# Kernel tuning notes

Measured on AMD Instinct MI355X. Metric: run time of the kernel, lower is better.

## Reference

```python
import jax, jax.numpy as jnp
import numpy as np

B, T, S, PD = 512, 2048, 16, 4

def setup_inputs() -> dict:
    key = jax.random.key(0)
    ks = jax.random.split(key, 10)
    w = lambda k, sh: (jax.random.normal(k, sh, dtype=jnp.float32) * 0.1)
    return {
        'z': jax.random.normal(ks[0], (B, T, S), dtype=jnp.float32),
        'p': jax.random.normal(ks[1], (B, T, PD), dtype=jnp.float32),
        'mu0': jnp.zeros((B, S), dtype=jnp.float32),
        'P0': jnp.full((B, S), 0.1, dtype=jnp.float32),  # cfg['kf_P0']
        'Wq1': w(ks[2], (PD, 64)), 'bq1': jnp.zeros((64,), jnp.float32),
        'Wq2': w(ks[3], (64, S)),  'bq2': jnp.zeros((S,), jnp.float32),
        'Wr1': w(ks[4], (PD, 64)), 'br1': jnp.zeros((64,), jnp.float32),
        'Wr2': w(ks[5], (64, S)),  'br2': jnp.zeros((S,), jnp.float32),
        'Wg1': w(ks[6], (PD, 32)), 'bg1': jnp.zeros((32,), jnp.float32),
        'Wg2': w(ks[7], (32, 1)),  'bg2': jnp.zeros((1,), jnp.float32),
    }

def _mlp(x, W1, b1, W2, b2):
    return jax.nn.relu(x @ W1 + b1) @ W2 + b2

def reference(z, p, mu0, P0, Wq1, bq1, Wq2, bq2, Wr1, br1, Wr2, br2, Wg1, bg1, Wg2, bg2):
    # z: [B,T,S], p: [B,T,PD]; scan over time with batched Kalman state.
    zT = jnp.swapaxes(z, 0, 1)  # [T,B,S]
    pT = jnp.swapaxes(p, 0, 1)  # [T,B,PD]

    def step(carry, inp):
        mu, P = carry            # [B,S], [B,S]
        z_t, p_t = inp           # [B,S], [B,PD]
        Q_t = jax.nn.softplus(_mlp(p_t, Wq1, bq1, Wq2, bq2)) + 1e-8
        R_t = jax.nn.softplus(_mlp(p_t, Wr1, br1, Wr2, br2)) + 1e-8
        P_pred = P + Q_t
        K = jnp.clip(P_pred / (P_pred + R_t), 1e-6, 0.95)
        gamma_t = jax.nn.sigmoid(_mlp(p_t, Wg1, bg1, Wg2, bg2))  # [B,1] (scalar per sample)
        mu_new = mu + gamma_t * (K * (z_t - mu))
        P_new = (1.0 - K) * P_pred
        return (mu_new, P_new), mu_new

    (mu_f, P_f), mus = jax.lax.scan(step, (mu0, P0), (zT, pT))
    return jnp.swapaxes(mus, 0, 1)  # [B,T,S]
```

## Files before the change

### kernel.cpp

```cpp
#include <hip/hip_runtime.h>
#include <hip/hip_fp16.h>
#include <stdint.h>
#include <math.h>

#define KB 512
#define KT 2048
#define KS 16
#define KPD 4
#define QT 512
#define NQ (KT / QT)
#define QSTR 515
#define HSTR 40

typedef _Float16 f16;
typedef _Float16 f16x8 __attribute__((ext_vector_type(8)));
typedef float f32x4 __attribute__((ext_vector_type(4)));

#define MFMA16(A, B, C) __builtin_amdgcn_mfma_f32_16x16x32_f16(A, B, C, 0, 0, 0)

__device__ __forceinline__ float softplus_f(float x) {
    float ax = fabsf(x);
    float e  = __expf(-ax);
    return fmaxf(x, 0.0f) + __logf(1.0f + e);
}
__device__ __forceinline__ float sigmoid_f(float x) {
    return __builtin_amdgcn_rcpf(1.0f + __expf(-x));
}
__device__ __forceinline__ float h2f_lo(uint32_t w) {
    return __half2float(__ushort_as_half((unsigned short)(w & 0xffffu)));
}
__device__ __forceinline__ float h2f_hi(uint32_t w) {
    return __half2float(__ushort_as_half((unsigned short)(w >> 16)));
}
__device__ __forceinline__ f16x8 zero8() {
    f16x8 v;
#pragma unroll
    for (int i = 0; i < 8; ++i) v[i] = (f16)0;
    return v;
}
__device__ __forceinline__ int spos(int t) { return t ^ ((t >> 5) & 31); }

__device__ __forceinline__ uint32_t pkrelu(float a, float b) {
    auto h = __builtin_amdgcn_cvt_pkrtz(fmaxf(a, 0.f), fmaxf(b, 0.f));
    uint32_t w; __builtin_memcpy(&w, &h, 4);
    return w;
}
__device__ __forceinline__ uint16_t f2h(float x) {
    return (uint16_t)__half_as_ushort(__float2half_rn(x));
}
__device__ __forceinline__ float h2f(uint16_t x) {
    return __half2float(__ushort_as_half((unsigned short)x));
}

__global__ __launch_bounds__(512, 2) void kalman_one(
    const float* __restrict__ z, const float* __restrict__ p,
    const float* __restrict__ mu0, const float* __restrict__ P0,
    const float* __restrict__ Wq1, const float* __restrict__ bq1,
    const float* __restrict__ Wq2, const float* __restrict__ bq2,
    const float* __restrict__ Wr1, const float* __restrict__ br1,
    const float* __restrict__ Wr2, const float* __restrict__ br2,
    const float* __restrict__ Wg1, const float* __restrict__ bg1,
    const float* __restrict__ Wg2, const float* __restrict__ bg2,
    float* __restrict__ out)
{
    __shared__ __align__(16) uint32_t QRl[KS * QSTR];
    __shared__ __align__(16) float    Gl[QT];
    __shared__ __align__(16) uint16_t Hs[8 * KS * HSTR];
    __shared__ __align__(16) uint16_t zsh[KS * QSTR];

    const int tid = threadIdx.x;
    const int wv = tid >> 6;
    const int l = tid & 63;
    const int g = l >> 4;
    const int c = l & 15;
    const int b = blockIdx.x;

    f16* __restrict__ Hw = reinterpret_cast<f16*>(Hs) + wv * (KS * HSTR);

    const float* __restrict__ zb = z + (size_t)b * KT * KS;
    const float* __restrict__ pb = p + (size_t)b * KT * KPD;
    float* __restrict__ ob = out + (size_t)b * KT * KS;

    f16x8 fA1[10];
#pragma unroll
    for (int m = 0; m < 10; ++m) {
        const float* W = (m < 4) ? (Wq1 + m * 16)
                       : (m < 8) ? (Wr1 + (m - 4) * 16)
                                 : (Wg1 + (m - 8) * 16);
        const int ld = (m < 8) ? 64 : 32;
        float w0 = W[0 * ld + c], w1 = W[1 * ld + c],
              w2 = W[2 * ld + c], w3 = W[3 * ld + c];
        f16x8 a = zero8();
        if (g == 0) { a[0] = (f16)w0; a[1] = (f16)w1; a[2] = (f16)w2; a[3] = (f16)w3; }
        fA1[m] = a;
    }
    f16x8 fA2[5];
#pragma unroll
    for (int i = 0; i < 4; ++i) {
        const float* W = (i < 2) ? Wq2 : Wr2;
        const int kb = (i & 1) * 32;
        f16x8 a;
#pragma unroll
        for (int j = 0; j < 8; ++j) a[j] = (f16)W[(kb + g * 8 + j) * 16 + c];
        fA2[i] = a;
    }
    {
        f16x8 a = zero8();
        if (c == 0) {
#pragma unroll
            for (int j = 0; j < 8; ++j) a[j] = (f16)Wg2[g * 8 + j];
        }
        fA2[4] = a;
    }
    const float bQ0 = bq2[g * 4 + 0], bQ1 = bq2[g * 4 + 1],
                bQ2 = bq2[g * 4 + 2], bQ3 = bq2[g * 4 + 3];
    const float bR0 = br2[g * 4 + 0], bR1 = br2[g * 4 + 1],
                bR2 = br2[g * 4 + 2], bR3 = br2[g * 4 + 3];
    const float bG = bg2[0];

    float muA = mu0[b * KS + wv],     PA = P0[b * KS + wv];
    float muB = mu0[b * KS + wv + 8], PB = P0[b * KS + wv + 8];

    auto scan_s = [&](int s, float& mu_q, float& P_q) {
        uint32_t qr[8];
        const uint32_t* qrow = QRl + (size_t)s * QSTR;
        float zvv[8], gvv[8];
#pragma unroll
        for (int i = 0; i < 8; ++i) {
            const int ps = spos(l * 8 + i);
            qr[i] = qrow[ps];
            zvv[i] = h2f(zsh[s * QSTR + ps]);
            gvv[i] = Gl[ps];
        }
        float c00 = 1.f, c01 = 0.f, c10 = 0.f, c11 = 1.f;
#pragma unroll
        for (int i = 0; i < 8; ++i) {
            float Q = h2f_lo(qr[i]), Rr = h2f_hi(qr[i]);
            float ta = fmaf(Q, c10, c00);
            float tb = fmaf(Q, c11, c01);
            float n10 = fmaf(Q + Rr, c10, c00);
            float n11 = fmaf(Q + Rr, c11, c01);
            c00 = Rr * ta; c01 = Rr * tb; c10 = n10; c11 = n11;
        }
        float rn = __builtin_amdgcn_rcpf(c11);
        float ma = c00 * rn, mb = c01 * rn, mc = c10 * rn;
#pragma unroll
        for (int r = 0; r < 6; ++r) {
            const int d = 1 << r;
            float pa = __shfl_up(ma, d);
            float pbv = __shfl_up(mb, d);
            float pc = __shfl_up(mc, d);
            float na = fmaf(ma, pa, mb * pc);
            float nb = fmaf(ma, pbv, mb);
            float nc = fmaf(mc, pa, pc);
            float nd = fmaf(mc, pbv, 1.f);
            float rr = __builtin_amdgcn_rcpf(nd);
            bool act = (l >= d);
            ma = act ? na * rr : ma;
            mb = act ? nb * rr : mb;
            mc = act ? nc * rr : mc;
        }
        float ea = __shfl_up(ma, 1);
        float eb = __shfl_up(mb, 1);
        float ec = __shfl_up(mc, 1);
        if (l == 0) { ea = 1.f; eb = 0.f; ec = 0.f; }
        float P = fmaf(ea, P_q, eb) * __builtin_amdgcn_rcpf(fmaf(ec, P_q, 1.f));

        float av[8], bw[8];
        float A = 1.f, Bv = 0.f;
#pragma unroll
        for (int i = 0; i < 8; ++i) {
            float Q = h2f_lo(qr[i]), Rr = h2f_hi(qr[i]);
            float Pp = P + Q;
            float K0 = Pp * __builtin_amdgcn_rcpf(Pp + Rr);
            float Kk = __builtin_amdgcn_fmed3f(K0, 1e-6f, 0.95f);
            float gk = gvv[i] * Kk;
            av[i] = 1.f - gk;
            bw[i] = gk * zvv[i];
            P = fmaf(-Kk, Pp, Pp);
            A = A * av[i];
            Bv = fmaf(av[i], Bv, bw[i]);
        }
        float P_end = __shfl(P, 63);
#pragma unroll
        for (int r = 0; r < 6; ++r) {
            const int d = 1 << r;
            float pA = __shfl_up(A, d);
            float pB = __shfl_up(Bv, d);
            float nA = A * pA;
            float nB = fmaf(A, pB, Bv);
            bool act = (l >= d);
            A  = act ? nA : A;
            Bv = act ? nB : Bv;
        }
        float eA = __shfl_up(A, 1);
        float eB = __shfl_up(Bv, 1);
        if (l == 0) { eA = 1.f; eB = 0.f; }
        float mu = fmaf(eA, mu_q, eB);
#pragma unroll
        for (int i = 0; i < 8; ++i) {
            mu = fmaf(av[i], mu, bw[i]);
            zsh[s * QSTR + spos(l * 8 + i)] = f2h(mu);
        }
        mu_q = __shfl(mu, 63);
        P_q = P_end;
    };

    for (int q = 0; q < NQ; ++q) {
        {
            const int trow = q * QT + wv * 64;
            const float4 pv = *reinterpret_cast<const float4*>(pb + (size_t)(trow + l) * KPD);

#pragma unroll
            for (int n = 0; n < 4; ++n) {
                f16x8 fBP;
                {
                    const int src = n * 16 + c;
                    float x = __shfl(pv.x, src);
                    float y = __shfl(pv.y, src);
                    float zz = __shfl(pv.z, src);
                    float w = __shfl(pv.w, src);
                    fBP = zero8();
                    if (g == 0) { fBP[0] = (f16)x; fBP[1] = (f16)y; fBP[2] = (f16)zz; fBP[3] = (f16)w; }
                }

                f32x4 aq; aq[0] = bQ0; aq[1] = bQ1; aq[2] = bQ2; aq[3] = bQ3;
                f32x4 ar; ar[0] = bR0; ar[1] = bR1; ar[2] = bR2; ar[3] = bR3;
                f32x4 ag; ag[0] = 0.f; ag[1] = 0.f; ag[2] = 0.f; ag[3] = 0.f;

                uint32_t* Hd = reinterpret_cast<uint32_t*>(Hw);

#pragma unroll
                for (int X = 0; X < 5; ++X) {
                    const int m0 = 2 * X, m1 = 2 * X + 1;
                    {
                        const float* bs = (m0 < 4) ? (bq1 + m0 * 16)
                                        : (m0 < 8) ? (br1 + (m0 - 4) * 16)
                                                   : (bg1 + (m0 - 8) * 16);
                        f32x4 acc;
                        acc[0] = bs[g * 4 + 0]; acc[1] = bs[g * 4 + 1];
                        acc[2] = bs[g * 4 + 2]; acc[3] = bs[g * 4 + 3];
                        acc = MFMA16(fA1[m0], fBP, acc);
                        Hd[c * 20 + g * 2 + 0] = pkrelu(acc[0], acc[1]);
                        Hd[c * 20 + g * 2 + 1] = pkrelu(acc[2], acc[3]);
                    }
                    {
                        const float* bs = (m1 < 4) ? (bq1 + m1 * 16)
                                        : (m1 < 8) ? (br1 + (m1 - 4) * 16)
                                                   : (bg1 + (m1 - 8) * 16);
                        f32x4 acc;
                        acc[0] = bs[g * 4 + 0]; acc[1] = bs[g * 4 + 1];
                        acc[2] = bs[g * 4 + 2]; acc[3] = bs[g * 4 + 3];
                        acc = MFMA16(fA1[m1], fBP, acc);
                        Hd[c * 20 + 8 + g * 2 + 0] = pkrelu(acc[0], acc[1]);
                        Hd[c * 20 + 8 + g * 2 + 1] = pkrelu(acc[2], acc[3]);
                    }
                    f16x8 fb = *reinterpret_cast<const f16x8*>(Hw + c * HSTR + g * 8);
                    if (X == 0)      aq = MFMA16(fA2[0], fb, aq);
                    else if (X == 1) aq = MFMA16(fA2[1], fb, aq);
                    else if (X == 2) ar = MFMA16(fA2[2], fb, ar);
                    else if (X == 3) ar = MFMA16(fA2[3], fb, ar);
                    else             ag = MFMA16(fA2[4], fb, ag);
                }

                const int tt = wv * 64 + n * 16 + c;
                const int ps = spos(tt);
#pragma unroll
                for (int i = 0; i < 4; ++i) {
                    float Qv = softplus_f(aq[i]) + 1e-8f;
                    float Rv = softplus_f(ar[i]) + 1e-8f;
                    auto pk = __builtin_amdgcn_cvt_pkrtz(Qv, Rv);
                    uint32_t w; __builtin_memcpy(&w, &pk, 4);
                    QRl[(size_t)(g * 4 + i) * QSTR + ps] = w;
                }
                if (g == 0)
                    Gl[ps] = sigmoid_f(ag[0] + bG);
            }

            const float4* zq = reinterpret_cast<const float4*>(zb + (size_t)q * QT * KS);
#pragma unroll
            for (int v = 0; v < 4; ++v) {
                int k = tid + 512 * v;
                float4 w = zq[k];
                int t = k >> 2, s0 = (k & 3) << 2;
                const int ps = spos(t);
                zsh[(s0 + 0) * QSTR + ps] = f2h(w.x);
                zsh[(s0 + 1) * QSTR + ps] = f2h(w.y);
                zsh[(s0 + 2) * QSTR + ps] = f2h(w.z);
                zsh[(s0 + 3) * QSTR + ps] = f2h(w.w);
            }
        }
        __syncthreads();

        scan_s(wv, muA, PA);
        scan_s(wv + 8, muB, PB);
        __syncthreads();

        {
            float* od = ob + (size_t)q * QT * KS;
#pragma unroll
            for (int v = 0; v < 4; ++v) {
                int k = tid + 512 * v;
                int t = k >> 2, s0 = (k & 3) << 2;
                const int ps = spos(t);
                float4 w;
                w.x = h2f(zsh[(s0 + 0) * QSTR + ps]);
                w.y = h2f(zsh[(s0 + 1) * QSTR + ps]);
                w.z = h2f(zsh[(s0 + 2) * QSTR + ps]);
                w.w = h2f(zsh[(s0 + 3) * QSTR + ps]);
                *reinterpret_cast<float4*>(od + 4 * (size_t)k) = w;
            }
        }
        __syncthreads();
    }
}

extern "C" void kernel_launch(void* const* d_in, const int* in_sizes, int n_in,
                              void* d_out, int out_size, void* d_ws, size_t ws_size,
                              hipStream_t stream) {
    const float* z   = (const float*)d_in[0];
    const float* p   = (const float*)d_in[1];
    const float* mu0 = (const float*)d_in[2];
    const float* P0  = (const float*)d_in[3];
    const float* Wq1 = (const float*)d_in[4];
    const float* bq1 = (const float*)d_in[5];
    const float* Wq2 = (const float*)d_in[6];
    const float* bq2 = (const float*)d_in[7];
    const float* Wr1 = (const float*)d_in[8];
    const float* br1 = (const float*)d_in[9];
    const float* Wr2 = (const float*)d_in[10];
    const float* br2 = (const float*)d_in[11];
    const float* Wg1 = (const float*)d_in[12];
    const float* bg1 = (const float*)d_in[13];
    const float* Wg2 = (const float*)d_in[14];
    const float* bg2 = (const float*)d_in[15];
    float* out = (float*)d_out;

    hipLaunchKernelGGL(kalman_one, dim3(KB), dim3(512), 0, stream,
                       z, p, mu0, P0, Wq1, bq1, Wq2, bq2,
                       Wr1, br1, Wr2, br2, Wg1, bg1, Wg2, bg2, out);
}
```

Baseline: 86.88 us.

## Add higher-occupancy kalman_fast kernel with LDS-staged MFMA weights and spill check

Adds a new kernel variant with launch bounds raised to four blocks per CU. It stages the fp16 first- and second-layer MLP weights in shared memory instead of keeping them in registers, so register pressure drops enough for the higher occupancy. The host queries the kernel's local (spill) memory size and falls back to the old kernel if the new one spills. The risks are extra LDS reads per MFMA, a larger shared-memory footprint that may itself cap occupancy, and a hipFuncGetAttributes call on every launch.

```diff
diff --git a/kernel.cpp b/kernel.cpp
--- a/kernel.cpp
+++ b/kernel.cpp
@@ -50,6 +50,296 @@
 }
 __device__ __forceinline__ float h2f(uint16_t x) {
     return __half2float(__ushort_as_half((unsigned short)x));
+}
+
+__global__ __launch_bounds__(512, 4) void kalman_fast(
+    const float* __restrict__ z, const float* __restrict__ p,
+    const float* __restrict__ mu0, const float* __restrict__ P0,
+    const float* __restrict__ Wq1, const float* __restrict__ bq1,
+    const float* __restrict__ Wq2, const float* __restrict__ bq2,
+    const float* __restrict__ Wr1, const float* __restrict__ br1,
+    const float* __restrict__ Wr2, const float* __restrict__ br2,
+    const float* __restrict__ Wg1, const float* __restrict__ bg1,
+    const float* __restrict__ Wg2, const float* __restrict__ bg2,
+    float* __restrict__ out)
+{
+    __shared__ __align__(16) uint32_t QRl[KS * QSTR];
+    __shared__ __align__(16) float    Gl[QT];
+    __shared__ __align__(16) uint16_t Hs[8 * KS * HSTR];
+    __shared__ __align__(16) uint16_t zsh[KS * QSTR];
+    __shared__ __align__(16) uint32_t WA1[10 * 16 * 2];
+    __shared__ __align__(16) uint32_t WA2[5 * 64 * 4];
+
+    const int tid = threadIdx.x;
+    const int wv = tid >> 6;
+    const int l = tid & 63;
+    const int g = l >> 4;
+    const int c = l & 15;
+    const int b = blockIdx.x;
+
+    f16* __restrict__ Hw = reinterpret_cast<f16*>(Hs) + wv * (KS * HSTR);
+
+    const float* __restrict__ zb = z + (size_t)b * KT * KS;
+    const float* __restrict__ pb = p + (size_t)b * KT * KPD;
+    float* __restrict__ ob = out + (size_t)b * KT * KS;
+
+    if (tid < 160) {
+        const int m = tid >> 4, cc = tid & 15;
+        const float* W = (m < 4) ? (Wq1 + m * 16)
+                       : (m < 8) ? (Wr1 + (m - 4) * 16)
+                                 : (Wg1 + (m - 8) * 16);
+        const int ld = (m < 8) ? 64 : 32;
+        f16 v[4];
+        v[0] = (f16)W[0 * ld + cc]; v[1] = (f16)W[1 * ld + cc];
+        v[2] = (f16)W[2 * ld + cc]; v[3] = (f16)W[3 * ld + cc];
+        uint32_t w0, w1;
+        __builtin_memcpy(&w0, &v[0], 4);
+        __builtin_memcpy(&w1, &v[2], 4);
+        WA1[(m * 16 + cc) * 2 + 0] = w0;
+        WA1[(m * 16 + cc) * 2 + 1] = w1;
+    }
+    if (tid < 320) {
+        const int i = tid >> 6, ll = tid & 63;
+        const int gg = ll >> 4, cc = ll & 15;
+        f16x8 a = zero8();
+        if (i < 4) {
+            const float* W = (i < 2) ? Wq2 : Wr2;
+            const int kb = (i & 1) * 32;
+#pragma unroll
+            for (int j = 0; j < 8; ++j) a[j] = (f16)W[(kb + gg * 8 + j) * 16 + cc];
+        } else if (cc == 0) {
+#pragma unroll
+            for (int j = 0; j < 8; ++j) a[j] = (f16)Wg2[gg * 8 + j];
+        }
+        uint4 t;
+        __builtin_memcpy(&t, &a, 16);
+        *reinterpret_cast<uint4*>(&WA2[(i * 64 + ll) * 4]) = t;
+    }
+
+    const float bQ0 = bq2[g * 4 + 0], bQ1 = bq2[g * 4 + 1],
+                bQ2 = bq2[g * 4 + 2], bQ3 = bq2[g * 4 + 3];
+    const float bR0 = br2[g * 4 + 0], bR1 = br2[g * 4 + 1],
+                bR2 = br2[g * 4 + 2], bR3 = br2[g * 4 + 3];
+    const float bG = bg2[0];
+
+    float muA = mu0[b * KS + wv],     PA = P0[b * KS + wv];
+    float muB = mu0[b * KS + wv + 8], PB = P0[b * KS + wv + 8];
+
+    __syncthreads();
+
+    auto scan_s = [&](int s, float& mu_q, float& P_q) {
+        uint32_t qr[8];
+        const uint32_t* qrow = QRl + (size_t)s * QSTR;
+        float zvv[8], gvv[8];
+#pragma unroll
+        for (int i = 0; i < 8; ++i) {
+            const int ps = spos(l * 8 + i);
+            qr[i] = qrow[ps];
+            zvv[i] = h2f(zsh[s * QSTR + ps]);
+            gvv[i] = Gl[ps];
+        }
+        float c00 = 1.f, c01 = 0.f, c10 = 0.f, c11 = 1.f;
+#pragma unroll
+        for (int i = 0; i < 8; ++i) {
+            float Q = h2f_lo(qr[i]), Rr = h2f_hi(qr[i]);
+            float ta = fmaf(Q, c10, c00);
+            float tb = fmaf(Q, c11, c01);
+            float n10 = fmaf(Q + Rr, c10, c00);
+            float n11 = fmaf(Q + Rr, c11, c01);
+            c00 = Rr * ta; c01 = Rr * tb; c10 = n10; c11 = n11;
+        }
+        float rn = __builtin_amdgcn_rcpf(c11);
+        float ma = c00 * rn, mb = c01 * rn, mc = c10 * rn;
+#pragma unroll
+        for (int r = 0; r < 6; ++r) {
+            const int d = 1 << r;
+            float pa = __shfl_up(ma, d);
+            float pbv = __shfl_up(mb, d);
+            float pc = __shfl_up(mc, d);
+            float na = fmaf(ma, pa, mb * pc);
+            float nb = fmaf(ma, pbv, mb);
+            float nc = fmaf(mc, pa, pc);
+            float nd = fmaf(mc, pbv, 1.f);
+            float rr = __builtin_amdgcn_rcpf(nd);
+            bool act = (l >= d);
+            ma = act ? na * rr : ma;
+            mb = act ? nb * rr : mb;
+            mc = act ? nc * rr : mc;
+        }
+        float ea = __shfl_up(ma, 1);
+        float eb = __shfl_up(mb, 1);
+        float ec = __shfl_up(mc, 1);
+        if (l == 0) { ea = 1.f; eb = 0.f; ec = 0.f; }
+        float P = fmaf(ea, P_q, eb) * __builtin_amdgcn_rcpf(fmaf(ec, P_q, 1.f));
+
+        float av[8], bw[8];
+        float A = 1.f, Bv = 0.f;
+#pragma unroll
+        for (int i = 0; i < 8; ++i) {
+            float Q = h2f_lo(qr[i]), Rr = h2f_hi(qr[i]);
+            float Pp = P + Q;
+            float K0 = Pp * __builtin_amdgcn_rcpf(Pp + Rr);
+            float Kk = __builtin_amdgcn_fmed3f(K0, 1e-6f, 0.95f);
+            float gk = gvv[i] * Kk;
+            av[i] = 1.f - gk;
+            bw[i] = gk * zvv[i];
+            P = fmaf(-Kk, Pp, Pp);
+            A = A * av[i];
+            Bv = fmaf(av[i], Bv, bw[i]);
+        }
+        float P_end = __shfl(P, 63);
+#pragma unroll
+        for (int r = 0; r < 6; ++r) {
+            const int d = 1 << r;
+            float pA = __shfl_up(A, d);
+            float pB = __shfl_up(Bv, d);
+            float nA = A * pA;
+            float nB = fmaf(A, pB, Bv);
+            bool act = (l >= d);
+            A  = act ? nA : A;
+            Bv = act ? nB : Bv;
+        }
+        float eA = __shfl_up(A, 1);
+        float eB = __shfl_up(Bv, 1);
+        if (l == 0) { eA = 1.f; eB = 0.f; }
+        float mu = fmaf(eA, mu_q, eB);
+#pragma unroll
+        for (int i = 0; i < 8; ++i) {
+            mu = fmaf(av[i], mu, bw[i]);
+            zsh[s * QSTR + spos(l * 8 + i)] = f2h(mu);
+        }
+        mu_q = __shfl(mu, 63);
+        P_q = P_end;
+    };
+
+    for (int q = 0; q < NQ; ++q) {
+        {
+            const int trow = q * QT + wv * 64;
+            const float4 pv = *reinterpret_cast<const float4*>(pb + (size_t)(trow + l) * KPD);
+
+#pragma unroll
+            for (int n = 0; n < 4; ++n) {
+                f16x8 fBP;
+                {
+                    const int src = n * 16 + c;
+                    float x = __shfl(pv.x, src);
+                    float y = __shfl(pv.y, src);
+                    float zz = __shfl(pv.z, src);
+                    float w = __shfl(pv.w, src);
+                    fBP = zero8();
+                    if (g == 0) { fBP[0] = (f16)x; fBP[1] = (f16)y; fBP[2] = (f16)zz; fBP[3] = (f16)w; }
+                }
+
+                f32x4 aq; aq[0] = bQ0; aq[1] = bQ1; aq[2] = bQ2; aq[3] = bQ3;
+                f32x4 ar; ar[0] = bR0; ar[1] = bR1; ar[2] = bR2; ar[3] = bR3;
+                f32x4 ag; ag[0] = 0.f; ag[1] = 0.f; ag[2] = 0.f; ag[3] = 0.f;
+
+                uint32_t* Hd = reinterpret_cast<uint32_t*>(Hw);
+
+#pragma unroll
+                for (int X = 0; X < 5; ++X) {
+                    const int m0 = 2 * X, m1 = 2 * X + 1;
+                    {
+                        const float* bs = (m0 < 4) ? (bq1 + m0 * 16)
+                                        : (m0 < 8) ? (br1 + (m0 - 4) * 16)
+                                                   : (bg1 + (m0 - 8) * 16);
+                        uint32_t p0 = WA1[(m0 * 16 + c) * 2 + 0];
+                        uint32_t p1 = WA1[(m0 * 16 + c) * 2 + 1];
+                        uint4 t;
+                        t.x = (g == 0) ? p0 : 0u;
+                        t.y = (g == 0) ? p1 : 0u;
+                        t.z = 0u; t.w = 0u;
+                        f16x8 A0;
+                        __builtin_memcpy(&A0, &t, 16);
+                        f32x4 acc;
+                        acc[0] = bs[g * 4 + 0]; acc[1] = bs[g * 4 + 1];
+                        acc[2] = bs[g * 4 + 2]; acc[3] = bs[g * 4 + 3];
+                        acc = MFMA16(A0, fBP, acc);
+                        Hd[c * 20 + g * 2 + 0] = pkrelu(acc[0], acc[1]);
+                        Hd[c * 20 + g * 2 + 1] = pkrelu(acc[2], acc[3]);
+                    }
+                    {
+                        const float* bs = (m1 < 4) ? (bq1 + m1 * 16)
+                                        : (m1 < 8) ? (br1 + (m1 - 4) * 16)
+                                                   : (bg1 + (m1 - 8) * 16);
+                        uint32_t p0 = WA1[(m1 * 16 + c) * 2 + 0];
+                        uint32_t p1 = WA1[(m1 * 16 + c) * 2 + 1];
+                        uint4 t;
+                        t.x = (g == 0) ? p0 : 0u;
+                        t.y = (g == 0) ? p1 : 0u;
+                        t.z = 0u; t.w = 0u;
+                        f16x8 A1;
+                        __builtin_memcpy(&A1, &t, 16);
+                        f32x4 acc;
+                        acc[0] = bs[g * 4 + 0]; acc[1] = bs[g * 4 + 1];
+                        acc[2] = bs[g * 4 + 2]; acc[3] = bs[g * 4 + 3];
+                        acc = MFMA16(A1, fBP, acc);
+                        Hd[c * 20 + 8 + g * 2 + 0] = pkrelu(acc[0], acc[1]);
+                        Hd[c * 20 + 8 + g * 2 + 1] = pkrelu(acc[2], acc[3]);
+                    }
+                    f16x8 fb = *reinterpret_cast<const f16x8*>(Hw + c * HSTR + g * 8);
+                    f16x8 A2;
+                    {
+                        uint4 t2 = *reinterpret_cast<const uint4*>(&WA2[(X * 64 + l) * 4]);
+                        __builtin_memcpy(&A2, &t2, 16);
+                    }
+                    if (X == 0)      aq = MFMA16(A2, fb, aq);
+                    else if (X == 1) aq = MFMA16(A2, fb, aq);
+                    else if (X == 2) ar = MFMA16(A2, fb, ar);
+                    else if (X == 3) ar = MFMA16(A2, fb, ar);
+                    else             ag = MFMA16(A2, fb, ag);
+                }
+
+                const int tt = wv * 64 + n * 16 + c;
+                const int ps = spos(tt);
+#pragma unroll
+                for (int i = 0; i < 4; ++i) {
+                    float Qv = softplus_f(aq[i]) + 1e-8f;
+                    float Rv = softplus_f(ar[i]) + 1e-8f;
+                    auto pk = __builtin_amdgcn_cvt_pkrtz(Qv, Rv);
+                    uint32_t w; __builtin_memcpy(&w, &pk, 4);
+                    QRl[(size_t)(g * 4 + i) * QSTR + ps] = w;
+                }
+                if (g == 0)
+                    Gl[ps] = sigmoid_f(ag[0] + bG);
+            }
+
+            const float4* zq = reinterpret_cast<const float4*>(zb + (size_t)q * QT * KS);
+#pragma unroll
+            for (int v = 0; v < 4; ++v) {
+                int k = tid + 512 * v;
+                float4 w = zq[k];
+                int t = k >> 2, s0 = (k & 3) << 2;
+                const int ps = spos(t);
+                zsh[(s0 + 0) * QSTR + ps] = f2h(w.x);
+                zsh[(s0 + 1) * QSTR + ps] = f2h(w.y);
+                zsh[(s0 + 2) * QSTR + ps] = f2h(w.z);
+                zsh[(s0 + 3) * QSTR + ps] = f2h(w.w);
+            }
+        }
+        __syncthreads();
+
+        scan_s(wv, muA, PA);
+        scan_s(wv + 8, muB, PB);
+        __syncthreads();
+
+        {
+            float* od = ob + (size_t)q * QT * KS;
+#pragma unroll
+            for (int v = 0; v < 4; ++v) {
+                int k = tid + 512 * v;
+                int t = k >> 2, s0 = (k & 3) << 2;
+                const int ps = spos(t);
+                float4 w;
+                w.x = h2f(zsh[(s0 + 0) * QSTR + ps]);
+                w.y = h2f(zsh[(s0 + 1) * QSTR + ps]);
+                w.z = h2f(zsh[(s0 + 2) * QSTR + ps]);
+                w.w = h2f(zsh[(s0 + 3) * QSTR + ps]);
+                *reinterpret_cast<float4*>(od + 4 * (size_t)k) = w;
+            }
+        }
+        __syncthreads();
+    }
 }
 
 __global__ __launch_bounds__(512, 2) void kalman_one(
@@ -336,7 +626,18 @@
     const float* bg2 = (const float*)d_in[15];
     float* out = (float*)d_out;
 
-    hipLaunchKernelGGL(kalman_one, dim3(KB), dim3(512), 0, stream,
-                       z, p, mu0, P0, Wq1, bq1, Wq2, bq2,
-                       Wr1, br1, Wr2, br2, Wg1, bg1, Wg2, bg2, out);
-}
+    hipFuncAttributes attr{};
+    bool use_fast = false;
+    if (hipFuncGetAttributes(&attr, (const void*)kalman_fast) == hipSuccess)
+        use_fast = (attr.localSizeBytes <= 16);
+
+    if (use_fast) {
+        hipLaunchKernelGGL(kalman_fast, dim3(KB), dim3(512), 0, stream,
+                           z, p, mu0, P0, Wq1, bq1, Wq2, bq2,
+                           Wr1, br1, Wr2, br2, Wg1, bg1, Wg2, bg2, out);
+    } else {
+        hipLaunchKernelGGL(kalman_one, dim3(KB), dim3(512), 0, stream,
+                           z, p, mu0, P0, Wq1, bq1, Wq2, bq2,
+                           Wr1, br1, Wr2, br2, Wg1, bg1, Wg2, bg2, out);
+    }
+}
```

After: 86.49 us. About the same (-0.4%).
